# Optimization experiments

Measured on AMD Instinct MI355X. Metric: run time of the kernel, lower is better.

Reference implementation:

```python
import jax, jax.numpy as jnp
import numpy as np

# E2M1 (FP4) representable magnitudes and rounding midpoints
LEVELS = jnp.array([0.0, 0.5, 1.0, 1.5, 2.0, 3.0, 4.0, 6.0], dtype=jnp.float32)
BOUNDS = jnp.array([0.25, 0.75, 1.25, 1.75, 2.5, 3.5, 5.0], dtype=jnp.float32)
E2M1_MAX = 6.0
EPS = 1e-12


def e2m1_block_quant_dequant(x, block_size):
    """Block-wise E2M1 fake-quantization along the last dim.

    Per block of `block_size` elements: scale = absmax / 6.0, then
    round-to-nearest onto the E2M1 grid {0,.5,1,1.5,2,3,4,6} (signed)
    and dequantize. Returns (dequantized x, per-block scales).
    """
    shape = x.shape
    nb = shape[-1] // block_size
    xb = x.reshape(*shape[:-1], nb, block_size)
    amax = jnp.max(jnp.abs(xb), axis=-1, keepdims=True)          # [..., nb, 1]
    scale = jnp.maximum(amax / E2M1_MAX, EPS)
    v = xb / scale
    mag = jnp.abs(v)
    # nearest E2M1 level: count how many rounding boundaries |v| exceeds
    idx = jnp.sum((mag[..., None] > BOUNDS).astype(jnp.int32), axis=-1)
    q = jnp.sign(v) * LEVELS[idx] * scale                        # dequantized
    return q.reshape(shape), scale[..., 0]


def setup_inputs() -> dict:
    key = jax.random.key(0)
    k1, k2, k3 = jax.random.split(key, 3)
    x = jax.random.normal(k1, (8, 1500, 1280), dtype=jnp.float32)
    weight = jax.random.normal(k2, (5120, 1280), dtype=jnp.float32) * 0.02
    bias = jax.random.normal(k3, (5120,), dtype=jnp.float32) * 0.01
    return {"x": x, "weight": weight, "bias": bias}


def reference(x, weight, bias):
    # activation quant (block_size_act = 32, along feature dim)
    x_q, _ = e2m1_block_quant_dequant(x, 32)
    # weight quant (block_size_w = 32, along in_features dim)
    w_q, scale_w = e2m1_block_quant_dequant(weight, 32)
    # F.linear: x @ W^T + b
    out = jnp.einsum('bsi,oi->bso', x_q, w_q) + bias
    return (out, scale_w)
```

## Files before the change

kernel.cpp:

```cpp
#include <hip/hip_runtime.h>
#include <hip/hip_fp16.h>


typedef _Float16 f16;
typedef _Float16 f16x8 __attribute__((ext_vector_type(8)));
typedef float f32x4 __attribute__((ext_vector_type(4)));

#define M_ROWS 12000
#define M_PAD  12032
#define N_COLS 5120
#define K_DIM  1280
#define KB     40
#define NTN    20
#define XBLK   7520

#define BAR()   asm volatile("s_barrier" ::: "memory")
#define VMCNT(N) asm volatile("s_waitcnt vmcnt(%0)" :: "i"(N) : "memory")
#define GLDS(gp, lp) __builtin_amdgcn_global_load_lds( \
    (const __attribute__((address_space(1))) unsigned*)(gp), \
    (__attribute__((address_space(3))) unsigned*)(lp), 16, 0, 0)

__device__ __forceinline__ float e2m1_level(float a) {
    float lv;
    if (a > 2.5f)       lv = (a > 3.5f) ? ((a > 5.0f) ? 6.0f : 4.0f) : 3.0f;
    else if (a > 1.25f) lv = (a > 1.75f) ? 2.0f : 1.5f;
    else                lv = (a > 0.75f) ? 1.0f : ((a > 0.25f) ? 0.5f : 0.0f);
    return lv;
}

__global__ __launch_bounds__(256) void quant_fused(const float* __restrict__ x,
                                                   f16* __restrict__ xq,
                                                   const float* __restrict__ w,
                                                   f16* __restrict__ wq,
                                                   float* __restrict__ scale_out) {
    int b = blockIdx.x;
    if (b < XBLK) {
        int t = b * 256 + threadIdx.x;
        int row = t / 160;
        int c8  = t % 160;
        f16x8 o;
        if (row < M_ROWS) {
            const float* p = x + (size_t)row * K_DIM + c8 * 8;
            float v[8];
            *(float4*)&v[0] = *(const float4*)p;
            *(float4*)&v[4] = *(const float4*)(p + 4);
            float am = 0.0f;
            #pragma unroll
            for (int i = 0; i < 8; ++i) am = fmaxf(am, fabsf(v[i]));
            am = fmaxf(am, __shfl_xor(am, 1));
            am = fmaxf(am, __shfl_xor(am, 2));
            float scale = fmaxf(am / 6.0f, 1e-12f);
            #pragma unroll
            for (int i = 0; i < 8; ++i) {
                float tq = v[i] / scale;
                float q  = copysignf(e2m1_level(fabsf(tq)), tq) * scale;
                o[i] = (f16)q;
            }
        } else {
            #pragma unroll
            for (int i = 0; i < 8; ++i) o[i] = (f16)0.0f;
        }
        *(f16x8*)(xq + (size_t)row * K_DIM + c8 * 8) = o;
    } else {
        int t = (b - XBLK) * 256 + threadIdx.x;
        int row = t / 160;
        int c8  = t % 160;
        const float* p = w + (size_t)row * K_DIM + c8 * 8;
        float v[8];
        *(float4*)&v[0] = *(const float4*)p;
        *(float4*)&v[4] = *(const float4*)(p + 4);
        float am = 0.0f;
        #pragma unroll
        for (int i = 0; i < 8; ++i) am = fmaxf(am, fabsf(v[i]));
        am = fmaxf(am, __shfl_xor(am, 1));
        am = fmaxf(am, __shfl_xor(am, 2));
        float scale = fmaxf(am / 6.0f, 1e-12f);
        if ((t & 3) == 0) scale_out[row * KB + (c8 >> 2)] = scale;
        f16x8 o;
        #pragma unroll
        for (int i = 0; i < 8; ++i) {
            float tq = v[i] / scale;
            float q  = copysignf(e2m1_level(fabsf(tq)), tq) * scale;
            o[i] = (f16)q;
        }
        *(f16x8*)(wq + (size_t)row * K_DIM + c8 * 8) = o;
    }
}


__device__ __forceinline__ void stage_half(const f16* __restrict__ g, f16* l, int tid) {
    #pragma unroll
    for (int s = 0; s < 2; ++s) {
        int j = s * 512 + tid;
        int r = j >> 3;
        int c = (j & 7) ^ (r & 7);
        GLDS(g + (size_t)r * K_DIM + c * 8, l + (size_t)j * 8);
    }
}

#define READ_A(dst, buf, rbase)                                                \
    _Pragma("unroll")                                                          \
    for (int fm = 0; fm < 4; ++fm) {                                           \
        dst[fm][0] = *(const f16x8*)&(buf)[((rbase) + fm * 16) * 64 + swz[0]]; \
        dst[fm][1] = *(const f16x8*)&(buf)[((rbase) + fm * 16) * 64 + swz[1]]; \
    }
#define READ_B(dst, buf, rbase)                                                \
    _Pragma("unroll")                                                          \
    for (int fn = 0; fn < 2; ++fn) {                                           \
        dst[fn][0] = *(const f16x8*)&(buf)[((rbase) + fn * 16) * 64 + swz[0]]; \
        dst[fn][1] = *(const f16x8*)&(buf)[((rbase) + fn * 16) * 64 + swz[1]]; \
    }
#define MFMA_Q(ma, mb, mo, no)                                                 \
    __builtin_amdgcn_s_setprio(1);                                             \
    _Pragma("unroll")                                                          \
    for (int fm = 0; fm < 4; ++fm)                                             \
        _Pragma("unroll")                                                      \
        for (int fn = 0; fn < 2; ++fn) {                                       \
            acc[fm + mo][fn + no] = __builtin_amdgcn_mfma_f32_16x16x32_f16(    \
                ma[fm][0], mb[fn][0], acc[fm + mo][fn + no], 0, 0, 0);         \
            acc[fm + mo][fn + no] = __builtin_amdgcn_mfma_f32_16x16x32_f16(    \
                ma[fm][1], mb[fn][1], acc[fm + mo][fn + no], 0, 0, 0);         \
        }                                                                      \
    __builtin_amdgcn_s_setprio(0);

template<bool SREST, int V4>
__device__ __forceinline__ void iter8(f16* A0, f16* B0, f16* A1, f16* B1,
                                      const f16* gA1, const f16* gA2,
                                      const f16* gB2, const f16* gB3,
                                      f32x4 (&acc)[8][4],
                                      int tid, int arow0, int brow0, const int (&swz)[2]) {
    f16x8 aLO[4][2], aHI[4][2], bLO[2][2], bHI[2][2];

    stage_half(gA1, A1, tid);
    READ_A(aLO, A0, arow0);
    READ_B(bLO, B0, brow0);
    MFMA_Q(aLO, bLO, 0, 0);
    BAR();
    stage_half(gA1 + 128 * K_DIM, A1 + 8192, tid);
    READ_B(bHI, B0, brow0 + 32);
    MFMA_Q(aLO, bHI, 0, 2);
    BAR();
    if (SREST) stage_half(gB2, B0, tid);
    READ_A(aHI, A0, arow0 + 64);
    MFMA_Q(aHI, bHI, 4, 2);
    BAR();
    if (SREST) stage_half(gA2, A0, tid);
    MFMA_Q(aHI, bLO, 4, 0);
    VMCNT(V4);
    BAR();
    if (SREST) stage_half(gA2 + 128 * K_DIM, A0 + 8192, tid);
    READ_A(aLO, A1, arow0);
    READ_B(bLO, B1, brow0);
    MFMA_Q(aLO, bLO, 0, 0);
    BAR();
    if (SREST) stage_half(gB2 + 128 * K_DIM, B0 + 8192, tid);
    READ_B(bHI, B1, brow0 + 32);
    MFMA_Q(aLO, bHI, 0, 2);
    BAR();
    if (SREST) stage_half(gB3, B1, tid);
    READ_A(aHI, A1, arow0 + 64);
    MFMA_Q(aHI, bHI, 4, 2);
    BAR();
    if (SREST) stage_half(gB3 + 128 * K_DIM, B1 + 8192, tid);
    MFMA_Q(aHI, bLO, 4, 0);
    if (SREST) VMCNT(4);
    BAR();
}

__global__ __launch_bounds__(512, 2) void gemm_kernel(const f16* __restrict__ A,
                                                      const f16* __restrict__ B,
                                                      const float* __restrict__ bias,
                                                      float* __restrict__ C) {
    extern __shared__ f16 sm[];
    int mt = blockIdx.x / NTN;
    int nt = blockIdx.x % NTN;

    int tid  = threadIdx.x;
    int lane = tid & 63;
    int wid  = tid >> 6;
    int wr   = wid >> 2;
    int wc   = wid & 3;
    int l15  = lane & 15;

    int swz[2] = { (((lane >> 4)    ) ^ (lane & 7)) * 8,
                   (((lane >> 4) + 4) ^ (lane & 7)) * 8 };
    int arow0 = wr * 128 + l15;
    int brow0 = wc * 64 + l15;

    const f16* gAb = A + (size_t)(mt * 256) * K_DIM;
    const f16* gBb = B + (size_t)(nt * 256) * K_DIM;

    f16* A0 = sm;
    f16* B0 = sm + 16384;
    f16* A1 = sm + 32768;
    f16* B1 = sm + 49152;

    f32x4 acc[8][4] = {};

    stage_half(gBb,               B0,        tid);
    stage_half(gAb,               A0,        tid);
    stage_half(gAb + 128 * K_DIM, A0 + 8192, tid);
    stage_half(gBb + 128 * K_DIM, B0 + 8192, tid);
    stage_half(gBb + 64,               B1,        tid);
    stage_half(gBb + 64 + 128 * K_DIM, B1 + 8192, tid);
    VMCNT(4);
    BAR();

    for (int i = 0; i < 9; ++i) {
        const f16* gA1 = gAb + (2 * i + 1) * 64;
        const f16* gA2 = gAb + (2 * i + 2) * 64;
        const f16* gB2 = gBb + (2 * i + 2) * 64;
        const f16* gB3 = gBb + (2 * i + 3) * 64;
        iter8<true, 4>(A0, B0, A1, B1, gA1, gA2, gB2, gB3,
                       acc, tid, arow0, brow0, swz);
    }
    iter8<false, 0>(A0, B0, A1, B1, gAb + 19 * 64, gAb, gBb, gBb,
                    acc, tid, arow0, brow0, swz);

    int crow0 = mt * 256 + wr * 128;
    int ccol  = nt * 256 + wc * 64 + l15;
    float bz[4];
    #pragma unroll
    for (int fn = 0; fn < 4; ++fn) bz[fn] = bias[ccol + fn * 16];

    #pragma unroll
    for (int fm = 0; fm < 8; ++fm) {
        #pragma unroll
        for (int j = 0; j < 4; ++j) {
            int row = crow0 + fm * 16 + (lane >> 4) * 4 + j;
            if (row < M_ROWS) {
                float* cp = C + (size_t)row * N_COLS + ccol;
                #pragma unroll
                for (int fn = 0; fn < 4; ++fn)
                    cp[fn * 16] = acc[fm][fn][j] + bz[fn];
            }
        }
    }
}

extern "C" void kernel_launch(void* const* d_in, const int* in_sizes, int n_in,
                              void* d_out, int out_size, void* d_ws, size_t ws_size,
                              hipStream_t stream) {
    const float* x      = (const float*)d_in[0];
    const float* weight = (const float*)d_in[1];
    const float* bias   = (const float*)d_in[2];
    float* out     = (float*)d_out;
    float* scale_w = (float*)d_out + (size_t)M_ROWS * N_COLS;

    f16* xq = (f16*)d_ws;
    f16* wq = (f16*)((char*)d_ws + (size_t)M_PAD * K_DIM * sizeof(f16));

    (void)hipFuncSetAttribute((const void*)gemm_kernel,
                              hipFuncAttributeMaxDynamicSharedMemorySize, 131072);

    {
        int wblocks = N_COLS * (K_DIM / 8) / 256;
        quant_fused<<<XBLK + wblocks, 256, 0, stream>>>(x, xq, weight, wq, scale_w);
    }
    {
        int grid = (M_PAD / 256) * (N_COLS / 256);
        gemm_kernel<<<grid, 512, 131072, stream>>>(xq, wq, bias, out);
    }
}
```

Baseline: 190.1 us.

## Restructure GEMM mainloop into 4-stage K=32 LDS ring with register double-buffering

Replaces the two-buffer K=64 schedule, which had eight barriers per iteration pair and interleaved quarter-tile MFMA groups, with a four-slot LDS ring of K=32 tiles. The next slice's fragments are prefetched into registers while the current slice's 32 MFMAs issue. Each K-step now needs one barrier plus a vmcnt wait, and the LDS swizzle changes to match the 32-wide rows. The aim is fewer barriers and deeper global-load prefetch. In exchange it holds more fragment registers, which may pressure occupancy at 512 threads with 2 blocks per CU.

After: 210.4 us. +10.7%, slower.

```diff
diff --git a/kernel.cpp b/kernel.cpp
--- a/kernel.cpp
+++ b/kernel.cpp
@@ -88,83 +88,43 @@
 }
 
 
-__device__ __forceinline__ void stage_half(const f16* __restrict__ g, f16* l, int tid) {
+__device__ __forceinline__ void stage32(const f16* __restrict__ g, f16* l, int tid) {
     #pragma unroll
     for (int s = 0; s < 2; ++s) {
         int j = s * 512 + tid;
-        int r = j >> 3;
-        int c = (j & 7) ^ (r & 7);
+        int r = j >> 2;
+        int c = (j & 3) ^ ((r >> 1) & 3);
         GLDS(g + (size_t)r * K_DIM + c * 8, l + (size_t)j * 8);
     }
 }
 
-#define READ_A(dst, buf, rbase)                                                \
-    _Pragma("unroll")                                                          \
-    for (int fm = 0; fm < 4; ++fm) {                                           \
-        dst[fm][0] = *(const f16x8*)&(buf)[((rbase) + fm * 16) * 64 + swz[0]]; \
-        dst[fm][1] = *(const f16x8*)&(buf)[((rbase) + fm * 16) * 64 + swz[1]]; \
-    }
-#define READ_B(dst, buf, rbase)                                                \
-    _Pragma("unroll")                                                          \
-    for (int fn = 0; fn < 2; ++fn) {                                           \
-        dst[fn][0] = *(const f16x8*)&(buf)[((rbase) + fn * 16) * 64 + swz[0]]; \
-        dst[fn][1] = *(const f16x8*)&(buf)[((rbase) + fn * 16) * 64 + swz[1]]; \
-    }
-#define MFMA_Q(ma, mb, mo, no)                                                 \
-    __builtin_amdgcn_s_setprio(1);                                             \
-    _Pragma("unroll")                                                          \
-    for (int fm = 0; fm < 4; ++fm)                                             \
-        _Pragma("unroll")                                                      \
-        for (int fn = 0; fn < 2; ++fn) {                                       \
-            acc[fm + mo][fn + no] = __builtin_amdgcn_mfma_f32_16x16x32_f16(    \
-                ma[fm][0], mb[fn][0], acc[fm + mo][fn + no], 0, 0, 0);         \
-            acc[fm + mo][fn + no] = __builtin_amdgcn_mfma_f32_16x16x32_f16(    \
-                ma[fm][1], mb[fn][1], acc[fm + mo][fn + no], 0, 0, 0);         \
-        }                                                                      \
+template<int VM, bool STG, bool RD>
+__device__ __forceinline__ void kt(const f16* RA, const f16* RB,
+                                   f16* SA, f16* SB,
+                                   const f16* gA3, const f16* gB3,
+                                   f16x8 (&ar)[8], f16x8 (&br)[4],
+                                   const f16x8 (&am)[8], const f16x8 (&bm)[4],
+                                   f32x4 (&acc)[8][4],
+                                   int tid, int arow0, int brow0, int swzc) {
+    if (VM == 4) VMCNT(4);
+    else if (VM == 0) VMCNT(0);
+    BAR();
+    if (STG) { stage32(gA3, SA, tid); stage32(gB3, SB, tid); }
+    if (RD) {
+        #pragma unroll
+        for (int fm = 0; fm < 8; ++fm)
+            ar[fm] = *(const f16x8*)&RA[(arow0 + fm * 16) * 32 + swzc];
+        #pragma unroll
+        for (int fn = 0; fn < 4; ++fn)
+            br[fn] = *(const f16x8*)&RB[(brow0 + fn * 16) * 32 + swzc];
+    }
+    __builtin_amdgcn_s_setprio(1);
+    #pragma unroll
+    for (int fm = 0; fm < 8; ++fm)
+        #pragma unroll
+        for (int fn = 0; fn < 4; ++fn)
+            acc[fm][fn] = __builtin_amdgcn_mfma_f32_16x16x32_f16(am[fm], bm[fn], acc[fm][fn], 0, 0, 0);
     __builtin_amdgcn_s_setprio(0);
-
-template<bool SREST, int V4>
-__device__ __forceinline__ void iter8(f16* A0, f16* B0, f16* A1, f16* B1,
-                                      const f16* gA1, const f16* gA2,
-                                      const f16* gB2, const f16* gB3,
-                                      f32x4 (&acc)[8][4],
-                                      int tid, int arow0, int brow0, const int (&swz)[2]) {
-    f16x8 aLO[4][2], aHI[4][2], bLO[2][2], bHI[2][2];
-
-    stage_half(gA1, A1, tid);
-    READ_A(aLO, A0, arow0);
-    READ_B(bLO, B0, brow0);
-    MFMA_Q(aLO, bLO, 0, 0);
-    BAR();
-    stage_half(gA1 + 128 * K_DIM, A1 + 8192, tid);
-    READ_B(bHI, B0, brow0 + 32);
-    MFMA_Q(aLO, bHI, 0, 2);
-    BAR();
-    if (SREST) stage_half(gB2, B0, tid);
-    READ_A(aHI, A0, arow0 + 64);
-    MFMA_Q(aHI, bHI, 4, 2);
-    BAR();
-    if (SREST) stage_half(gA2, A0, tid);
-    MFMA_Q(aHI, bLO, 4, 0);
-    VMCNT(V4);
-    BAR();
-    if (SREST) stage_half(gA2 + 128 * K_DIM, A0 + 8192, tid);
-    READ_A(aLO, A1, arow0);
-    READ_B(bLO, B1, brow0);
-    MFMA_Q(aLO, bLO, 0, 0);
-    BAR();
-    if (SREST) stage_half(gB2 + 128 * K_DIM, B0 + 8192, tid);
-    READ_B(bHI, B1, brow0 + 32);
-    MFMA_Q(aLO, bHI, 0, 2);
-    BAR();
-    if (SREST) stage_half(gB3, B1, tid);
-    READ_A(aHI, A1, arow0 + 64);
-    MFMA_Q(aHI, bHI, 4, 2);
-    BAR();
-    if (SREST) stage_half(gB3 + 128 * K_DIM, B1 + 8192, tid);
-    MFMA_Q(aHI, bLO, 4, 0);
-    if (SREST) VMCNT(4);
-    BAR();
 }
 
 __global__ __launch_bounds__(512, 2) void gemm_kernel(const f16* __restrict__ A,
@@ -182,40 +142,52 @@
     int wc   = wid & 3;
     int l15  = lane & 15;
 
-    int swz[2] = { (((lane >> 4)    ) ^ (lane & 7)) * 8,
-                   (((lane >> 4) + 4) ^ (lane & 7)) * 8 };
+    int swzc  = (((lane >> 4) ^ ((l15 >> 1) & 3)) << 3);
     int arow0 = wr * 128 + l15;
     int brow0 = wc * 64 + l15;
 
     const f16* gAb = A + (size_t)(mt * 256) * K_DIM;
     const f16* gBb = B + (size_t)(nt * 256) * K_DIM;
 
-    f16* A0 = sm;
-    f16* B0 = sm + 16384;
-    f16* A1 = sm + 32768;
-    f16* B1 = sm + 49152;
+    f16* A0 = sm;              f16* B0 = sm + 8192;
+    f16* A1 = sm + 16384;      f16* B1 = sm + 24576;
+    f16* A2 = sm + 32768;      f16* B2 = sm + 40960;
+    f16* A3 = sm + 49152;      f16* B3 = sm + 57344;
 
     f32x4 acc[8][4] = {};
-
-    stage_half(gBb,               B0,        tid);
-    stage_half(gAb,               A0,        tid);
-    stage_half(gAb + 128 * K_DIM, A0 + 8192, tid);
-    stage_half(gBb + 128 * K_DIM, B0 + 8192, tid);
-    stage_half(gBb + 64,               B1,        tid);
-    stage_half(gBb + 64 + 128 * K_DIM, B1 + 8192, tid);
-    VMCNT(4);
+    f16x8 a0[8], b0[4], a1[8], b1[4];
+
+    stage32(gAb,      A0, tid); stage32(gBb,      B0, tid);
+    stage32(gAb + 32, A1, tid); stage32(gBb + 32, B1, tid);
+    stage32(gAb + 64, A2, tid); stage32(gBb + 64, B2, tid);
+    VMCNT(8);
     BAR();
-
-    for (int i = 0; i < 9; ++i) {
-        const f16* gA1 = gAb + (2 * i + 1) * 64;
-        const f16* gA2 = gAb + (2 * i + 2) * 64;
-        const f16* gB2 = gBb + (2 * i + 2) * 64;
-        const f16* gB3 = gBb + (2 * i + 3) * 64;
-        iter8<true, 4>(A0, B0, A1, B1, gA1, gA2, gB2, gB3,
-                       acc, tid, arow0, brow0, swz);
-    }
-    iter8<false, 0>(A0, B0, A1, B1, gAb + 19 * 64, gAb, gBb, gBb,
-                    acc, tid, arow0, brow0, swz);
+    #pragma unroll
+    for (int fm = 0; fm < 8; ++fm)
+        a0[fm] = *(const f16x8*)&A0[(arow0 + fm * 16) * 32 + swzc];
+    #pragma unroll
+    for (int fn = 0; fn < 4; ++fn)
+        b0[fn] = *(const f16x8*)&B0[(brow0 + fn * 16) * 32 + swzc];
+
+    for (int it = 0; it < 9; ++it) {
+        int t = 4 * it;
+        kt<4, true, true>(A1, B1, A3, B3, gAb + (t + 3) * 32, gBb + (t + 3) * 32,
+                          a1, b1, a0, b0, acc, tid, arow0, brow0, swzc);
+        kt<4, true, true>(A2, B2, A0, B0, gAb + (t + 4) * 32, gBb + (t + 4) * 32,
+                          a0, b0, a1, b1, acc, tid, arow0, brow0, swzc);
+        kt<4, true, true>(A3, B3, A1, B1, gAb + (t + 5) * 32, gBb + (t + 5) * 32,
+                          a1, b1, a0, b0, acc, tid, arow0, brow0, swzc);
+        kt<4, true, true>(A0, B0, A2, B2, gAb + (t + 6) * 32, gBb + (t + 6) * 32,
+                          a0, b0, a1, b1, acc, tid, arow0, brow0, swzc);
+    }
+    kt<4, true, true>(A1, B1, A3, B3, gAb + 39 * 32, gBb + 39 * 32,
+                      a1, b1, a0, b0, acc, tid, arow0, brow0, swzc);
+    kt<4, false, true>(A2, B2, A2, B2, gAb, gBb,
+                       a0, b0, a1, b1, acc, tid, arow0, brow0, swzc);
+    kt<0, false, true>(A3, B3, A3, B3, gAb, gBb,
+                       a1, b1, a0, b0, acc, tid, arow0, brow0, swzc);
+    kt<-1, false, false>(A0, B0, A0, B0, gAb, gBb,
+                         a0, b0, a1, b1, acc, tid, arow0, brow0, swzc);
 
     int crow0 = mt * 256 + wr * 128;
     int ccol  = nt * 256 + wc * 64 + l15;
```
